# Kernel optimization log

Hardware: AMD Instinct MI355X
Metric: run time of the kernel (lower is better)

## Reference

```python
import jax, jax.numpy as jnp
import numpy as np

N_NODES = 100000
N_EDGES = 1600000
IN_DIM = 128
HID = 128
N_CLASSES = 10
N_GRAPHS = 64


def setup_inputs() -> dict:
    key = jax.random.key(0)
    ks = jax.random.split(key, 12)
    x = jax.random.normal(ks[0], (N_NODES, IN_DIM), dtype=jnp.float32)
    edge_index = jax.random.randint(ks[1], (2, N_EDGES), 0, N_NODES, dtype=jnp.int64)
    batch = jnp.sort(jax.random.randint(ks[2], (N_NODES,), 0, N_GRAPHS, dtype=jnp.int64))
    s = 1.0 / np.sqrt(HID)
    W_gcn = jax.random.uniform(ks[3], (IN_DIM, HID), jnp.float32, -s, s)
    b_gcn = jnp.zeros((HID,), jnp.float32)
    w_ih = jax.random.uniform(ks[4], (4 * HID, HID), jnp.float32, -s, s)
    w_hh = jax.random.uniform(ks[5], (4 * HID, HID), jnp.float32, -s, s)
    b_ih = jax.random.uniform(ks[6], (4 * HID,), jnp.float32, -s, s)
    b_hh = jax.random.uniform(ks[7], (4 * HID,), jnp.float32, -s, s)
    W_fc = jax.random.uniform(ks[8], (N_CLASSES, HID), jnp.float32, -s, s)
    b_fc = jax.random.uniform(ks[9], (N_CLASSES,), jnp.float32, -s, s)
    return dict(x=x, edge_index=edge_index, batch=batch, W_gcn=W_gcn, b_gcn=b_gcn,
                w_ih=w_ih, w_hh=w_hh, b_ih=b_ih, b_hh=b_hh, W_fc=W_fc, b_fc=b_fc)


def _gcn_conv(x, edge_index, W, b):
    # PyG GCNConv: add self-loops, symmetric norm D^-1/2 (A+I) D^-1/2, then bias.
    row, col = edge_index[0], edge_index[1]
    ones = jnp.ones((edge_index.shape[1],), x.dtype)
    deg = jax.ops.segment_sum(ones, col, num_segments=N_NODES) + 1.0  # +1 for self-loop
    dinv = jax.lax.rsqrt(deg)
    xt = x @ W  # [N, HID]
    norm = dinv[row] * dinv[col]  # [E]
    agg = jax.ops.segment_sum(xt[row] * norm[:, None], col, num_segments=N_NODES)
    agg = agg + xt * (dinv * dinv)[:, None]  # self-loop contribution
    return agg + b


def _lstm(seq, w_ih, w_hh, b_ih, b_hh):
    # torch LSTM gate order: i, f, g, o
    def step(carry, x_t):
        h, c = carry
        gates = x_t @ w_ih.T + h @ w_hh.T + b_ih + b_hh
        i, f, g, o = jnp.split(gates, 4)
        c = jax.nn.sigmoid(f) * c + jax.nn.sigmoid(i) * jnp.tanh(g)
        h = jax.nn.sigmoid(o) * jnp.tanh(c)
        return (h, c), h
    h0 = jnp.zeros((HID,), seq.dtype)
    (_, _), hs = jax.lax.scan(step, (h0, h0), seq)
    return hs  # [T, HID]


def reference(x, edge_index, batch, W_gcn, b_gcn, w_ih, w_hh, b_ih, b_hh, W_fc, b_fc):
    h = jax.nn.relu(_gcn_conv(x, edge_index, W_gcn, b_gcn))
    # dropout is identity at inference
    sums = jax.ops.segment_sum(h, batch, num_segments=N_GRAPHS)
    cnt = jax.ops.segment_sum(jnp.ones((N_NODES,), h.dtype), batch, num_segments=N_GRAPHS)
    pooled = sums / jnp.maximum(cnt, 1.0)[:, None]  # [G, HID]
    hs = _lstm(pooled, w_ih, w_hh, b_ih, b_hh)  # [G, HID]
    return hs @ W_fc.T + b_fc  # [G, N_CLASSES]
```

## Files before the change

### kernel.cpp

```cpp
#include <hip/hip_runtime.h>
#include <hip/hip_fp16.h>
#include <math.h>

#if __has_builtin(__builtin_amdgcn_cvt_pk_f32_fp8) && __has_builtin(__builtin_amdgcn_cvt_pk_fp8_f32)
#define HAS_FP8_CVT 1
#else
#include <hip/hip_fp8.h>
#endif

#define NNODES 100000
#define NEDGES 1600000
#define DIM 128
#define NG 64
#define GATE 512
#define SCAN_NB 98
#define FILL_NPASS 4
#define BUCKET ((NNODES + FILL_NPASS - 1) / FILL_NPASS)

#define HG 128
#define HW 25024
#define HSMEM (HW * 4)

typedef _Float16 half8_t __attribute__((ext_vector_type(8)));
typedef float f32x4 __attribute__((ext_vector_type(4)));
typedef float f32x2_t __attribute__((ext_vector_type(2)));

__device__ __forceinline__ unsigned char f32_to_fp8(float v) {
#ifdef HAS_FP8_CVT
    return (unsigned char)(__builtin_amdgcn_cvt_pk_fp8_f32(v, v, 0, false) & 0xFF);
#else
    __hip_fp8_e4m3 h(v); return h.__x;
#endif
}
__device__ __forceinline__ void fp8x4_acc(unsigned w, float* acc) {
#ifdef HAS_FP8_CVT
    f32x2_t lo = __builtin_amdgcn_cvt_pk_f32_fp8((int)w, false);
    f32x2_t hi = __builtin_amdgcn_cvt_pk_f32_fp8((int)w, true);
    acc[0] += lo[0]; acc[1] += lo[1]; acc[2] += hi[0]; acc[3] += hi[1];
#else
    __hip_fp8_e4m3 h;
#pragma unroll
    for (int q = 0; q < 4; ++q) { h.__x = (w >> (8 * q)) & 0xFF; acc[q] += (float)h; }
#endif
}

__device__ __forceinline__ float sigf(float x) {
    return __builtin_amdgcn_rcpf(1.0f + __expf(-x));
}
__device__ __forceinline__ float tanhfast(float x) {
    float e = __expf(2.0f * x);
    return 1.0f - 2.0f * __builtin_amdgcn_rcpf(e + 1.0f);
}

__global__ __launch_bounds__(1024) void k_deghist(const int* __restrict__ ei, unsigned* __restrict__ partial) {
    extern __shared__ unsigned hist[];
    int tid = threadIdx.x;
    for (int i = tid; i < HW; i += 1024) hist[i] = 0u;
    __syncthreads();
    int e0 = blockIdx.x * (NEDGES / HG);
    int e1 = e0 + (NEDGES / HG);
    for (int e = e0 + tid; e < e1; e += 1024) {
        int col = ei[NEDGES + e];
        atomicAdd(&hist[col >> 2], 1u << ((col & 3) * 8));
    }
    __syncthreads();
    unsigned* dst = partial + (size_t)blockIdx.x * HW;
    for (int i = tid; i < HW; i += 1024) dst[i] = hist[i];
}

__global__ __launch_bounds__(256) void k_deg(const int* __restrict__ ei, int* __restrict__ deg) {
    int e = blockIdx.x * 256 + threadIdx.x;
    if (e < NEDGES) atomicAdd(&deg[ei[NEDGES + e]], 1);
}

__global__ __launch_bounds__(256) void k_degred2(const unsigned* __restrict__ partial, unsigned* __restrict__ pre8,
                                                 int* __restrict__ deg, float* __restrict__ dinv) {
    int w = blockIdx.x * 256 + threadIdx.x;
    if (w >= NNODES / 4) return;
    unsigned s = 0;
    for (int b = 0; b < HG; ++b) {
        pre8[(size_t)b * HW + w] = s;
        s += partial[(size_t)b * HW + w];
    }
    int4 d;
    d.x = s & 255; d.y = (s >> 8) & 255; d.z = (s >> 16) & 255; d.w = (int)(s >> 24);
    ((int4*)deg)[w] = d;
    float4 dv;
    dv.x = rsqrtf((float)d.x + 1.f);
    dv.y = rsqrtf((float)d.y + 1.f);
    dv.z = rsqrtf((float)d.z + 1.f);
    dv.w = rsqrtf((float)d.w + 1.f);
    ((float4*)dinv)[w] = dv;
}

__global__ __launch_bounds__(256) void k_dinv(const int* __restrict__ deg, float* __restrict__ dinv) {
    int n = blockIdx.x * 256 + threadIdx.x;
    if (n < NNODES) dinv[n] = rsqrtf((float)deg[n] + 1.0f);
}

__global__ __launch_bounds__(1024) void k_scan1(const int* __restrict__ deg, int* __restrict__ row_ptr,
                                                int* __restrict__ bsum) {
    __shared__ int ls[1024];
    int tid = threadIdx.x;
    int n = blockIdx.x * 1024 + tid;
    int v = (n < NNODES) ? deg[n] : 0;
    ls[tid] = v;
    __syncthreads();
    for (int off = 1; off < 1024; off <<= 1) {
        int t = (tid >= off) ? ls[tid - off] : 0;
        __syncthreads();
        ls[tid] += t;
        __syncthreads();
    }
    if (n < NNODES) row_ptr[n] = ls[tid] - v;
    if (tid == 1023) bsum[blockIdx.x] = ls[1023];
}

__global__ __launch_bounds__(128) void k_scan2(int* __restrict__ bsum, int* __restrict__ row_ptr,
                                               const int* __restrict__ batch, int* __restrict__ start) {
    __shared__ int ls[128];
    int tid = threadIdx.x;
    int v = (tid < SCAN_NB) ? bsum[tid] : 0;
    ls[tid] = v;
    __syncthreads();
    for (int off = 1; off < 128; off <<= 1) {
        int t = (tid >= off) ? ls[tid - off] : 0;
        __syncthreads();
        ls[tid] += t;
        __syncthreads();
    }
    if (tid < SCAN_NB) bsum[tid] = ls[tid] - v;
    if (tid == 127) row_ptr[NNODES] = ls[127];
    if (tid <= NG) {
        int lo = 0, hi = NNODES;
        while (lo < hi) {
            int mid = (lo + hi) >> 1;
            if (batch[mid] < tid) lo = mid + 1; else hi = mid;
        }
        start[tid] = lo;
    }
}

__global__ __launch_bounds__(1024) void k_scan3(int* __restrict__ row_ptr, const int* __restrict__ bsum,
                                                int* __restrict__ cursor) {
    int n = blockIdx.x * 1024 + threadIdx.x;
    if (n < NNODES) {
        int rp = row_ptr[n] + bsum[blockIdx.x];
        row_ptr[n] = rp;
        cursor[n] = rp;
    }
}

__global__ __launch_bounds__(1024) void k_fill2(const int* __restrict__ ei, const int* __restrict__ row_ptr,
                                                const unsigned* __restrict__ pre8, int* __restrict__ adj, int b0) {
    __shared__ unsigned lh[BUCKET / 4];
    int tid = threadIdx.x;
    for (int i = tid; i < BUCKET / 4; i += 1024) lh[i] = 0u;
    __syncthreads();
    const unsigned* myPre = pre8 + (size_t)blockIdx.x * HW;
    int e0 = blockIdx.x * (NEDGES / HG);
    int e1 = e0 + (NEDGES / HG);
    for (int e = e0 + tid; e < e1; e += 1024) {
        int col = ei[NEDGES + e];
        if (col >= b0 && col < b0 + BUCKET) {
            int row = ei[e];
            int lc = col - b0;
            unsigned old = atomicAdd(&lh[lc >> 2], 1u << ((lc & 3) * 8));
            int local = (old >> ((lc & 3) * 8)) & 0xFF;
            int base = row_ptr[col] + (int)((myPre[col >> 2] >> ((col & 3) * 8)) & 0xFF);
            adj[base + local] = row;
        }
    }
}

__global__ __launch_bounds__(256) void k_fillb(const int* __restrict__ ei, int* __restrict__ cursor,
                                               int* __restrict__ adj, int b0) {
    int e = blockIdx.x * 256 + threadIdx.x;
    if (e < NEDGES) {
        int col = ei[NEDGES + e];
        if (col >= b0 && col < b0 + BUCKET) {
            int row = ei[e];
            int pos = atomicAdd(&cursor[col], 1);
            adj[pos] = row;
        }
    }
}

__global__ __launch_bounds__(256) void k_wprep(const float* __restrict__ W_gcn, const float* __restrict__ w_hh,
                                               __half* __restrict__ Wt, __half* __restrict__ whh16) {
    int t = blockIdx.x * 256 + threadIdx.x;
    if (t < GATE * DIM) {
        whh16[t] = __float2half(w_hh[t]);
    } else {
        int idx = t - GATE * DIM;
        if (idx < DIM * DIM) {
            int d = idx >> 7, k = idx & 127;
            Wt[idx] = __float2half(W_gcn[k * DIM + d]);
        }
    }
}

__global__ __launch_bounds__(256) void k_gemmm(const float* __restrict__ x, const __half* __restrict__ Wt,
                                               const float* __restrict__ dinv, unsigned char* __restrict__ yf8) {
    int tid = threadIdx.x;
    int wt = tid >> 6, lane = tid & 63;
    int lr = lane & 15, kgrp = lane >> 4;
    int rb = blockIdx.x * 64 + wt * 16;

    int rowA = rb + lr;
    if (rowA >= NNODES) rowA = NNODES - 1;
    const float4* x4 = (const float4*)x;

    f32x4 acc[8];
#pragma unroll
    for (int ct = 0; ct < 8; ++ct) acc[ct] = (f32x4){0.f, 0.f, 0.f, 0.f};

#pragma unroll
    for (int c = 0; c < 4; ++c) {
        int kb = c * 32 + kgrp * 8;
        float4 v0 = x4[(size_t)rowA * 32 + (kb >> 2)];
        float4 v1 = x4[(size_t)rowA * 32 + (kb >> 2) + 1];
        half8_t a;
        a[0] = (_Float16)v0.x; a[1] = (_Float16)v0.y; a[2] = (_Float16)v0.z; a[3] = (_Float16)v0.w;
        a[4] = (_Float16)v1.x; a[5] = (_Float16)v1.y; a[6] = (_Float16)v1.z; a[7] = (_Float16)v1.w;
#pragma unroll
        for (int ct = 0; ct < 8; ++ct) {
            int col = ct * 16 + lr;
            half8_t b = *(const half8_t*)(Wt + (size_t)col * DIM + kb);
            acc[ct] = __builtin_amdgcn_mfma_f32_16x16x32_f16(a, b, acc[ct], 0, 0, 0);
        }
    }

    int rowbase = rb + kgrp * 4;
    float dv[4];
    bool ok[4];
#pragma unroll
    for (int r = 0; r < 4; ++r) {
        int row = rowbase + r;
        ok[r] = row < NNODES;
        dv[r] = ok[r] ? dinv[row] : 0.f;
    }
#pragma unroll
    for (int ct = 0; ct < 8; ++ct) {
#pragma unroll
        for (int r = 0; r < 4; ++r) {
            if (ok[r])
                yf8[(size_t)(rowbase + r) * DIM + ct * 16 + lr] = f32_to_fp8(acc[ct][r] * dv[r]);
        }
    }
}

__global__ __launch_bounds__(256) void k_gpool(const int* __restrict__ row_ptr, const int* __restrict__ adj,
                                               const uint2* __restrict__ Y, const float* __restrict__ dinv,
                                               const float* __restrict__ bias, const int* __restrict__ batch,
                                               float* __restrict__ sums) {
    __shared__ float red[16][132];
    __shared__ int gid[16];
    int tid = threadIdx.x;
    int sl = tid >> 4;
    int l = tid & 15;
    int n = blockIdx.x * 16 + sl;

    int s = row_ptr[n], e = row_ptr[n + 1];
    float acc[8];
#pragma unroll
    for (int q = 0; q < 8; ++q) acc[q] = 0.f;
    {
        uint2 v = Y[(size_t)n * 16 + l];
        fp8x4_acc(v.x, acc);
        fp8x4_acc(v.y, acc + 4);
    }
    int i = s;
    for (; i + 3 < e; i += 4) {
        int r0 = adj[i], r1 = adj[i + 1], r2 = adj[i + 2], r3 = adj[i + 3];
        uint2 a0 = Y[(size_t)r0 * 16 + l];
        uint2 a1 = Y[(size_t)r1 * 16 + l];
        uint2 a2 = Y[(size_t)r2 * 16 + l];
        uint2 a3 = Y[(size_t)r3 * 16 + l];
        fp8x4_acc(a0.x, acc); fp8x4_acc(a0.y, acc + 4);
        fp8x4_acc(a1.x, acc); fp8x4_acc(a1.y, acc + 4);
        fp8x4_acc(a2.x, acc); fp8x4_acc(a2.y, acc + 4);
        fp8x4_acc(a3.x, acc); fp8x4_acc(a3.y, acc + 4);
    }
    for (; i < e; ++i) {
        uint2 a0 = Y[(size_t)adj[i] * 16 + l];
        fp8x4_acc(a0.x, acc); fp8x4_acc(a0.y, acc + 4);
    }

    float dv = dinv[n];
#pragma unroll
    for (int q = 0; q < 8; ++q) {
        float v = dv * acc[q] + bias[l * 8 + q];
        red[sl][l * 8 + q] = fmaxf(v, 0.f);
    }
    if (l == 0) gid[sl] = batch[n];
    __syncthreads();

    if (tid < DIM) {
        int d = tid;
        float a = 0.f;
        int g = gid[0];
        for (int s2 = 0; s2 < 16; ++s2) {
            int gs = gid[s2];
            if (gs != g) {
                if (a != 0.f) atomicAdd(&sums[g * DIM + d], a);
                a = 0.f; g = gs;
            }
            a += red[s2][d];
        }
        if (a != 0.f) atomicAdd(&sums[g * DIM + d], a);
    }
}

__global__ __launch_bounds__(512) void k_xgate(const float* __restrict__ sums, const int* __restrict__ start,
                                               const float* __restrict__ w_ih, const float* __restrict__ b_ih,
                                               const float* __restrict__ b_hh, float* __restrict__ xg) {
    __shared__ float4 p4[DIM / 4];
    int t = blockIdx.x, j = threadIdx.x;
    if (j < DIM) {
        int c = start[t + 1] - start[t];
        float inv = 1.0f / fmaxf((float)c, 1.0f);
        ((float*)p4)[j] = sums[t * DIM + j] * inv;
    }
    __syncthreads();
    const float4* w4 = (const float4*)(w_ih + (size_t)j * DIM);
    float acc = b_ih[j] + b_hh[j];
#pragma unroll
    for (int kk = 0; kk < 32; ++kk) {
        float4 w = w4[kk];
        float4 p = p4[kk];
        acc += w.x * p.x + w.y * p.y + w.z * p.z + w.w * p.w;
    }
    xg[t * GATE + j] = acc;
}

__global__ __launch_bounds__(512) void k_lstmm(const float* __restrict__ xg, const __half* __restrict__ whh16,
                                               const float* __restrict__ Wfc, const float* __restrict__ bfc,
                                               float* __restrict__ out) {
    __shared__ __half h2h[DIM];
    __shared__ float gates[GATE];
    __shared__ __half hsh[NG * DIM];
    int tid = threadIdx.x;
    int wid = tid >> 6, lane = tid & 63;
    int lr = lane & 15, kg = lane >> 4;
    int colbase = wid * 64;

    half8_t bf[4][4];
#pragma unroll
    for (int ct = 0; ct < 4; ++ct)
#pragma unroll
        for (int ks = 0; ks < 4; ++ks)
            bf[ct][ks] = *(const half8_t*)(whh16 + (size_t)(colbase + ct * 16 + lr) * DIM + ks * 32 + kg * 8);

    if (tid < DIM) h2h[tid] = __float2half(0.f);
    float c = 0.f;
    float xc[4], xn[4];
#pragma unroll
    for (int ct = 0; ct < 4; ++ct) xc[ct] = xg[colbase + ct * 16 + lr];
    __syncthreads();

    for (int t = 0; t < NG; ++t) {
        half8_t a[4];
#pragma unroll
        for (int ks = 0; ks < 4; ++ks) {
            half8_t av = {};
            if (lr == 0) av = *(const half8_t*)(h2h + ks * 32 + kg * 8);
            a[ks] = av;
        }
        f32x4 acc[4];
#pragma unroll
        for (int ct = 0; ct < 4; ++ct) {
            f32x4 z = (f32x4){0.f, 0.f, 0.f, 0.f};
            if (lane < 16) z[0] = xc[ct];
            acc[ct] = z;
#pragma unroll
            for (int ks = 0; ks < 4; ++ks)
                acc[ct] = __builtin_amdgcn_mfma_f32_16x16x32_f16(a[ks], bf[ct][ks], acc[ct], 0, 0, 0);
        }
        int tn = (t + 1 < NG) ? t + 1 : t;
#pragma unroll
        for (int ct = 0; ct < 4; ++ct) xn[ct] = xg[tn * GATE + colbase + ct * 16 + lr];
        if (lane < 16) {
#pragma unroll
            for (int ct = 0; ct < 4; ++ct) gates[colbase + ct * 16 + lane] = acc[ct][0];
        }
        __syncthreads();
        if (tid < DIM) {
            float gi = gates[tid], gf = gates[DIM + tid], gg = gates[2 * DIM + tid], go = gates[3 * DIM + tid];
            c = sigf(gf) * c + sigf(gi) * tanhfast(gg);
            float hn = sigf(go) * tanhfast(c);
            h2h[tid] = __float2half(hn);
            hsh[t * DIM + tid] = __float2half(hn);
        }
#pragma unroll
        for (int ct = 0; ct < 4; ++ct) xc[ct] = xn[ct];
        __syncthreads();
    }

    for (int o = tid; o < NG * 10; o += 512) {
        int t = o / 10, cls = o - t * 10;
        const __half2* hv = (const __half2*)(hsh + t * DIM);
        float acc = bfc[cls];
#pragma unroll
        for (int kk = 0; kk < 64; ++kk) {
            float2 hf = __half22float2(hv[kk]);
            acc += hf.x * Wfc[cls * DIM + 2 * kk] + hf.y * Wfc[cls * DIM + 2 * kk + 1];
        }
        out[o] = acc;
    }
}

extern "C" void kernel_launch(void* const* d_in, const int* in_sizes, int n_in,
                              void* d_out, int out_size, void* d_ws, size_t ws_size,
                              hipStream_t stream) {
    const float* x     = (const float*)d_in[0];
    const int*   ei    = (const int*)d_in[1];
    const int*   batch = (const int*)d_in[2];
    const float* W_gcn = (const float*)d_in[3];
    const float* b_gcn = (const float*)d_in[4];
    const float* w_ih  = (const float*)d_in[5];
    const float* w_hh  = (const float*)d_in[6];
    const float* b_ih  = (const float*)d_in[7];
    const float* b_hh  = (const float*)d_in[8];
    const float* W_fc  = (const float*)d_in[9];
    const float* b_fc  = (const float*)d_in[10];
    float* out = (float*)d_out;

    char* ws = (char*)d_ws;
    unsigned char* yf8 = (unsigned char*)ws;
    unsigned* pre8 = (unsigned*)(ws + (size_t)NNODES * DIM);
    __half* wt16  = (__half*)(ws + (size_t)NNODES * DIM * 2);
    unsigned* partial = (unsigned*)(ws + (size_t)NNODES * DIM * 2 + (1 << 16));
    float*  dinv  = (float*)(ws + (size_t)NNODES * DIM * 4);
    float*  sums  = dinv + 100096;
    float*  xg    = sums + NG * DIM;
    int*    deg   = (int*)(xg + NG * GATE);
    int*    row_ptr = deg + 100096;
    int*    cursor  = row_ptr + 100096;
    int*    adj     = cursor + 100096;
    int*    start   = adj + NEDGES;
    int*    bsum    = start + 128;
    __half* whh16   = (__half*)(bsum + 128);

    hipMemsetAsync(sums, 0, NG * DIM * sizeof(float), stream);

    bool hist_ok = hipFuncSetAttribute((const void*)k_deghist,
                                       hipFuncAttributeMaxDynamicSharedMemorySize,
                                       HSMEM) == hipSuccess;
    if (hist_ok) {
        k_deghist<<<HG, 1024, HSMEM, stream>>>(ei, partial);
        k_degred2<<<(NNODES / 4 + 255) / 256, 256, 0, stream>>>(partial, pre8, deg, dinv);
    } else {
        hipMemsetAsync(deg, 0, NNODES * sizeof(int), stream);
        k_deg<<<(NEDGES + 255) / 256, 256, 0, stream>>>(ei, deg);
        k_dinv<<<(NNODES + 255) / 256, 256, 0, stream>>>(deg, dinv);
    }
    k_scan1<<<SCAN_NB, 1024, 0, stream>>>(deg, row_ptr, bsum);
    k_scan2<<<1, 128, 0, stream>>>(bsum, row_ptr, batch, start);
    k_scan3<<<SCAN_NB, 1024, 0, stream>>>(row_ptr, bsum, cursor);
    if (hist_ok) {
        for (int p = 0; p < FILL_NPASS; ++p)
            k_fill2<<<HG, 1024, 0, stream>>>(ei, row_ptr, pre8, adj, p * BUCKET);
    } else {
        for (int p = 0; p < FILL_NPASS; ++p)
            k_fillb<<<(NEDGES + 255) / 256, 256, 0, stream>>>(ei, cursor, adj, p * BUCKET);
    }
    k_wprep<<<(GATE * DIM + DIM * DIM + 255) / 256, 256, 0, stream>>>(W_gcn, w_hh, wt16, whh16);
    k_gemmm<<<(NNODES + 63) / 64, 256, 0, stream>>>(x, wt16, dinv, yf8);
    k_gpool<<<NNODES / 16, 256, 0, stream>>>(row_ptr, adj, (const uint2*)yf8, dinv, b_gcn, batch, sums);
    k_xgate<<<NG, 512, 0, stream>>>(sums, start, w_ih, b_ih, b_hh, xg);
    k_lstmm<<<1, 512, 0, stream>>>(xg, whh16, W_fc, b_fc, out);
}
```

Baseline: 236.2 us.

## Restructure LSTM kernel to compute gates in-register with one barrier per step

The serial LSTM kernel now runs with 4 waves instead of 8. Each wave owns matching i/f/g/o column tiles for two hidden units per lane, so the cell update happens directly from MFMA accumulators without a shared-memory gates buffer. Double-buffering the hidden state allows a single __syncthreads per timestep instead of two. This shortens the 64-step serial critical path, at the cost of more MFMA work per wave and higher register pressure from holding 32 weight fragments.

Result: slower. 247.4 us (+4.7%).

```diff
diff --git a/kernel.cpp b/kernel.cpp
--- a/kernel.cpp
+++ b/kernel.cpp
@@ -334,70 +334,81 @@
     xg[t * GATE + j] = acc;
 }
 
-__global__ __launch_bounds__(512) void k_lstmm(const float* __restrict__ xg, const __half* __restrict__ whh16,
-                                               const float* __restrict__ Wfc, const float* __restrict__ bfc,
-                                               float* __restrict__ out) {
-    __shared__ __half h2h[DIM];
-    __shared__ float gates[GATE];
+__global__ __launch_bounds__(256, 1) void k_lstmm(const float* __restrict__ xg, const __half* __restrict__ whh16,
+                                                  const float* __restrict__ Wfc, const float* __restrict__ bfc,
+                                                  float* __restrict__ out) {
+    __shared__ __half h2h[2][DIM];
     __shared__ __half hsh[NG * DIM];
     int tid = threadIdx.x;
     int wid = tid >> 6, lane = tid & 63;
     int lr = lane & 15, kg = lane >> 4;
-    int colbase = wid * 64;
-
-    half8_t bf[4][4];
-#pragma unroll
-    for (int ct = 0; ct < 4; ++ct)
-#pragma unroll
-        for (int ks = 0; ks < 4; ++ks)
-            bf[ct][ks] = *(const half8_t*)(whh16 + (size_t)(colbase + ct * 16 + lr) * DIM + ks * 32 + kg * 8);
-
-    if (tid < DIM) h2h[tid] = __float2half(0.f);
-    float c = 0.f;
-    float xc[4], xn[4];
-#pragma unroll
-    for (int ct = 0; ct < 4; ++ct) xc[ct] = xg[colbase + ct * 16 + lr];
+
+    float4 bfr[8][4];
+#pragma unroll
+    for (int ti = 0; ti < 8; ++ti) {
+#pragma unroll
+        for (int ks = 0; ks < 4; ++ks) {
+            const __half* p = whh16 + (size_t)((wid + 4 * ti) * 16 + lr) * DIM + ks * 32 + kg * 8;
+            asm volatile("global_load_dwordx4 %0, %1, off" : "=v"(bfr[ti][ks]) : "v"(p));
+        }
+    }
+    asm volatile("s_waitcnt vmcnt(0)" ::: "memory");
+    __builtin_amdgcn_sched_barrier(0);
+
+    if (tid < DIM) { h2h[0][tid] = __float2half(0.f); }
+    float c1 = 0.f, c2 = 0.f;
+    float xc[8], xn[8];
+    if (lane < 16) {
+#pragma unroll
+        for (int ti = 0; ti < 8; ++ti) xc[ti] = xg[(wid + 4 * ti) * 16 + lr];
+    }
+    int j1 = wid * 16 + lr;
+    int j2 = (wid + 4) * 16 + lr;
     __syncthreads();
 
     for (int t = 0; t < NG; ++t) {
+        const __half* hb = h2h[t & 1];
         half8_t a[4];
 #pragma unroll
         for (int ks = 0; ks < 4; ++ks) {
             half8_t av = {};
-            if (lr == 0) av = *(const half8_t*)(h2h + ks * 32 + kg * 8);
+            if (lr == 0) av = *(const half8_t*)(hb + ks * 32 + kg * 8);
             a[ks] = av;
         }
-        f32x4 acc[4];
-#pragma unroll
-        for (int ct = 0; ct < 4; ++ct) {
+        f32x4 acc[8];
+#pragma unroll
+        for (int ti = 0; ti < 8; ++ti) {
             f32x4 z = (f32x4){0.f, 0.f, 0.f, 0.f};
-            if (lane < 16) z[0] = xc[ct];
-            acc[ct] = z;
-#pragma unroll
-            for (int ks = 0; ks < 4; ++ks)
-                acc[ct] = __builtin_amdgcn_mfma_f32_16x16x32_f16(a[ks], bf[ct][ks], acc[ct], 0, 0, 0);
+            if (lane < 16) z[0] = xc[ti];
+            acc[ti] = z;
+#pragma unroll
+            for (int ks = 0; ks < 4; ++ks) {
+                union { float4 f; half8_t h; } u; u.f = bfr[ti][ks];
+                acc[ti] = __builtin_amdgcn_mfma_f32_16x16x32_f16(a[ks], u.h, acc[ti], 0, 0, 0);
+            }
         }
         int tn = (t + 1 < NG) ? t + 1 : t;
-#pragma unroll
-        for (int ct = 0; ct < 4; ++ct) xn[ct] = xg[tn * GATE + colbase + ct * 16 + lr];
         if (lane < 16) {
 #pragma unroll
-            for (int ct = 0; ct < 4; ++ct) gates[colbase + ct * 16 + lane] = acc[ct][0];
+            for (int ti = 0; ti < 8; ++ti) xn[ti] = xg[tn * GATE + (wid + 4 * ti) * 16 + lr];
+            float gi = acc[0][0], gf = acc[2][0], gg = acc[4][0], go = acc[6][0];
+            c1 = sigf(gf) * c1 + sigf(gi) * tanhfast(gg);
+            float hn1 = sigf(go) * tanhfast(c1);
+            gi = acc[1][0]; gf = acc[3][0]; gg = acc[5][0]; go = acc[7][0];
+            c2 = sigf(gf) * c2 + sigf(gi) * tanhfast(gg);
+            float hn2 = sigf(go) * tanhfast(c2);
+            __half h1 = __float2half(hn1), h2 = __float2half(hn2);
+            h2h[(t + 1) & 1][j1] = h1;
+            h2h[(t + 1) & 1][j2] = h2;
+            hsh[t * DIM + j1] = h1;
+            hsh[t * DIM + j2] = h2;
+#pragma unroll
+            for (int ti = 0; ti < 8; ++ti) xc[ti] = xn[ti];
         }
         __syncthreads();
-        if (tid < DIM) {
-            float gi = gates[tid], gf = gates[DIM + tid], gg = gates[2 * DIM + tid], go = gates[3 * DIM + tid];
-            c = sigf(gf) * c + sigf(gi) * tanhfast(gg);
-            float hn = sigf(go) * tanhfast(c);
-            h2h[tid] = __float2half(hn);
-            hsh[t * DIM + tid] = __float2half(hn);
-        }
-#pragma unroll
-        for (int ct = 0; ct < 4; ++ct) xc[ct] = xn[ct];
-        __syncthreads();
-    }
-
-    for (int o = tid; o < NG * 10; o += 512) {
+    }
+
+    for (int o = tid; o < NG * 10; o += 256) {
         int t = o / 10, cls = o - t * 10;
         const __half2* hv = (const __half2*)(hsh + t * DIM);
         float acc = bfc[cls];
@@ -469,5 +480,5 @@
     k_gemmm<<<(NNODES + 63) / 64, 256, 0, stream>>>(x, wt16, dinv, yf8);
     k_gpool<<<NNODES / 16, 256, 0, stream>>>(row_ptr, adj, (const uint2*)yf8, dinv, b_gcn, batch, sums);
     k_xgate<<<NG, 512, 0, stream>>>(sums, start, w_ih, b_ih, b_hh, xg);
-    k_lstmm<<<1, 512, 0, stream>>>(xg, whh16, W_fc, b_fc, out);
-}
+    k_lstmm<<<1, 256, 0, stream>>>(xg, whh16, W_fc, b_fc, out);
+}
```
